# Kernel optimization log

Hardware: AMD Instinct MI355X
Metric: run time of the kernel (lower is better)

Reference implementation:

```python
import jax, jax.numpy as jnp
from jax import lax
import numpy as np

B, C_IN, IMG = 32, 4, 224
FH = FW = IMG // 8  # 28: three stride-2 maxpools
NA = 4
SCORE_T, IOU_T, MAXP = 0.7, 0.3, 10
EPS = 1e-5


def conv2d(x, w, b, pad):
    y = lax.conv_general_dilated(x, w, (1, 1), [(pad, pad), (pad, pad)],
                                 dimension_numbers=('NCHW', 'OIHW', 'NCHW'))
    return y + b[None, :, None, None]


def bn_eval(x, g, b):
    # eval-mode BN with running_mean=0, running_var=1 (fresh model), eps=1e-5
    return x * (g / jnp.sqrt(1.0 + EPS))[None, :, None, None] + b[None, :, None, None]


def maxpool2(x):
    return lax.reduce_window(x, -jnp.inf, lax.max, (1, 1, 2, 2), (1, 1, 2, 2), 'VALID')


def make_anchors():
    ys = (jnp.arange(FH) + 0.5) / FH
    xs = (jnp.arange(FW) + 0.5) / FW
    cy, cx = jnp.meshgrid(ys, xs, indexing='ij')
    cxy = jnp.stack([cx, cy], -1)  # [H,W,2], matches loop order y,x then anchor
    sizes = jnp.array([[16., 16.], [32., 32.], [64., 64.], [128., 128.]], jnp.float32) / 224.0
    a = jnp.concatenate([jnp.broadcast_to(cxy[:, :, None, :], (FH, FW, NA, 2)),
                         jnp.broadcast_to(sizes[None, None], (FH, FW, NA, 2))], -1)
    return a.reshape(-1, 4)  # [H*W*NA, 4] = [3136, 4]


def decode_boxes(anchors, offsets):
    centers = anchors[..., :2] + offsets[..., :2] * 0.1
    sizes = anchors[..., 2:] * jnp.exp(offsets[..., 2:] * 0.2)
    boxes = jnp.concatenate([centers - sizes / 2, centers + sizes / 2], -1)
    return jnp.clip(boxes, 0.0, 1.0)


def nms_single(boxes, scores):
    # greedy NMS, fixed MAXP iterations (== max_proposals_per_image cap)
    N = scores.shape[0]
    s0 = jnp.where(scores > SCORE_T, scores, -jnp.inf)  # score-threshold filter
    areas = (boxes[:, 2] - boxes[:, 0]) * (boxes[:, 3] - boxes[:, 1])
    idx_all = jnp.arange(N)

    def body(s, _):
        i = jnp.argmax(s)
        ok = s[i] > -jnp.inf
        bi = boxes[i]
        xx1 = jnp.maximum(bi[0], boxes[:, 0]); yy1 = jnp.maximum(bi[1], boxes[:, 1])
        xx2 = jnp.minimum(bi[2], boxes[:, 2]); yy2 = jnp.minimum(bi[3], boxes[:, 3])
        inter = jnp.clip(xx2 - xx1, 0.0) * jnp.clip(yy2 - yy1, 0.0)
        iou = inter / (areas[i] + areas - inter)
        sup = (iou > IOU_T) | (idx_all == i)
        s_next = jnp.where(ok & sup, -jnp.inf, s)
        return s_next, (jnp.where(ok, i, 0), ok)

    _, (idxs, oks) = lax.scan(body, s0, None, length=MAXP)
    return idxs, oks  # [MAXP] int32, [MAXP] bool


def _forward(x, r1w, r1b, g1, b1, r2w, r2b, g2, b2, r3w, r3b, g3, b3, rpw, rpb,
             clsw, clsb, regw, regb, c1w, c1b, cg1, cb1, c2w, c2b, cg2, cb2,
             fc1w, fc1b, fc2w, fc2b, fc3w, fc3b, fc4w, fc4b):
    Bsz = x.shape[0]
    # --- Stage 1: lightweight RPN ---
    h = maxpool2(jax.nn.relu(bn_eval(conv2d(x, r1w, r1b, 1), g1, b1)))
    h = maxpool2(jax.nn.relu(bn_eval(conv2d(h, r2w, r2b, 1), g2, b2)))
    h = maxpool2(jax.nn.relu(bn_eval(conv2d(h, r3w, r3b, 1), g3, b3)))
    h = jax.nn.relu(conv2d(h, rpw, rpb, 1))
    cls = conv2d(h, clsw, clsb, 0).transpose(0, 2, 3, 1).reshape(Bsz, -1, 2)
    reg = conv2d(h, regw, regb, 0).transpose(0, 2, 3, 1).reshape(Bsz, -1, 4)
    anchors = make_anchors()
    probs = jax.nn.softmax(cls, -1)[..., 1]        # [B,N] objectness
    boxes = decode_boxes(anchors[None], reg)       # [B,N,4]
    # --- proposal selection: score threshold + greedy NMS + top-10 cap ---
    idxs, oks = jax.vmap(nms_single)(boxes, probs)  # [B,10]
    okf = oks.astype(boxes.dtype)
    kept_boxes = jax.vmap(lambda b, i: b[i])(boxes, idxs) * okf[..., None]
    kept_scores = jax.vmap(lambda s, i: s[i])(probs, idxs) * okf
    has_prop = (probs > SCORE_T).any(-1)           # [B]
    # --- Stage 2: CLM classifier (applied to the full image, as in original) ---
    f = jax.nn.relu(bn_eval(conv2d(x, c1w, c1b, 1), cg1, cb1))
    f = jax.nn.relu(bn_eval(conv2d(f, c2w, c2b, 1), cg2, cb2))
    # AdaptiveAvgPool2d((7,7)) on 224x224 -> mean over 32x32 blocks
    f = f.reshape(Bsz, 128, 7, 32, 7, 32).mean(axis=(3, 5)).reshape(Bsz, -1)
    f = jax.nn.relu(f @ fc1w + fc1b)
    f = jax.nn.relu(f @ fc2w + fc2b)
    f = jax.nn.relu(f @ fc3w + fc3b)
    logits = f @ fc4w + fc4b
    bg = jnp.array([1.0, 0.0], logits.dtype)
    final = jnp.where(has_prop[:, None], logits, bg[None])
    return final, kept_boxes, kept_scores, oks


def setup_inputs() -> dict:
    key = jax.random.key(0)
    ks = iter(jax.random.split(key, 64))

    def conv_w(o, i, k):
        return jax.random.normal(next(ks), (o, i, k, k), jnp.float32) * float(np.sqrt(2.0 / (i * k * k)))

    def lin_w(i, o):
        return jax.random.normal(next(ks), (i, o), jnp.float32) * float(1.0 / np.sqrt(i))

    return {
        'x': jax.random.normal(next(ks), (B, C_IN, IMG, IMG), jnp.float32),
        'r1w': conv_w(32, 4, 3), 'r1b': jnp.zeros(32), 'g1': jnp.ones(32), 'b1': jnp.zeros(32),
        'r2w': conv_w(64, 32, 3), 'r2b': jnp.zeros(64), 'g2': jnp.ones(64), 'b2': jnp.zeros(64),
        'r3w': conv_w(128, 64, 3), 'r3b': jnp.zeros(128), 'g3': jnp.ones(128), 'b3': jnp.zeros(128),
        'rpw': conv_w(256, 128, 3), 'rpb': jnp.zeros(256),
        'clsw': conv_w(8, 256, 1), 'clsb': jnp.zeros(8),
        'regw': conv_w(16, 256, 1), 'regb': jnp.zeros(16),
        'c1w': conv_w(64, 4, 3), 'c1b': jnp.zeros(64), 'cg1': jnp.ones(64), 'cb1': jnp.zeros(64),
        'c2w': conv_w(128, 64, 3), 'c2b': jnp.zeros(128), 'cg2': jnp.ones(128), 'cb2': jnp.zeros(128),
        'fc1w': lin_w(6272, 512), 'fc1b': jnp.zeros(512),
        'fc2w': lin_w(512, 256), 'fc2b': jnp.zeros(256),
        'fc3w': lin_w(256, 128), 'fc3b': jnp.zeros(128),
        'fc4w': lin_w(128, 2), 'fc4b': jnp.zeros(2),
    }


def reference(x, r1w, r1b, g1, b1, r2w, r2b, g2, b2, r3w, r3b, g3, b3, rpw, rpb,
              clsw, clsb, regw, regb, c1w, c1b, cg1, cb1, c2w, c2b, cg2, cb2,
              fc1w, fc1b, fc2w, fc2b, fc3w, fc3b, fc4w, fc4b):
    return _forward(x, r1w, r1b, g1, b1, r2w, r2b, g2, b2, r3w, r3b, g3, b3, rpw, rpb,
                    clsw, clsb, regw, regb, c1w, c1b, cg1, cb1, c2w, c2b, cg2, cb2,
                    fc1w, fc1b, fc2w, fc2b, fc3w, fc3b, fc4w, fc4b)
```

## Files before the change

### kernel.cpp

```cpp
#include <hip/hip_runtime.h>
#include <math.h>

constexpr int NANCH = 3136;
constexpr float SCORE_T = 0.7f;
constexpr float IOU_T = 0.3f;
constexpr int MAXP = 10;

typedef unsigned short u16;
typedef __attribute__((ext_vector_type(8))) short short8x;
typedef __attribute__((ext_vector_type(4))) float f32x4;

__device__ inline u16 f2bf(float f) {
  unsigned u = __builtin_bit_cast(unsigned, f);
  u += 0x7fffu + ((u >> 16) & 1u);
  return (u16)(u >> 16);
}
__device__ inline float bf2f(u16 h) {
  unsigned u = ((unsigned)h) << 16;
  return __builtin_bit_cast(float, u);
}

__global__ __launch_bounds__(256) void w1prep_k(const float* __restrict__ w,
                                                u16* __restrict__ hi, u16* __restrict__ lo,
                                                int COUT) {
  const int i = blockIdx.x * 256 + threadIdx.x;
  if (i >= COUT * 64) return;
  const int k = i & 63, co = i >> 6;
  float v = 0.f;
  if (k < 36) { const int tap = k >> 2, cin = k & 3; v = w[co * 36 + cin * 9 + tap]; }
  const u16 h = f2bf(v);
  hi[i] = h;
  lo[i] = f2bf(v - bf2f(h));
}

template<int MODE>
__global__ __launch_bounds__(256) void c1mfma_k(
    const float* __restrict__ x,
    const u16* __restrict__ wfh, const u16* __restrict__ wfl,
    const float* __restrict__ bias, const float* __restrict__ gamma,
    const float* __restrict__ beta,
    u16* __restrict__ outhi, u16* __restrict__ outlo) {
  constexpr int COUT = MODE ? 32 : 64;
  constexpr int NF   = MODE ? 2 : 4;
  constexpr int PS   = MODE ? 136 : 72;
  __shared__ u16 s_patch[64 * PS];
  __shared__ u16 s_wh[COUT * 72];
  __shared__ u16 s_wl[MODE ? COUT * 72 : 8];
  __shared__ float s_raw[4 * 6 * 18];
  __shared__ float s_pool[MODE ? 4 * 16 * 17 : 1];
  __shared__ u16 s_out[MODE ? 8 : 64 * 72];

  const int tid = threadIdx.x, lane = tid & 63, w = tid >> 6;
  const int lr = lane & 15, lg = lane >> 4;
  const int img = blockIdx.z;
  const int x0 = blockIdx.x * 16, y0 = blockIdx.y * 4;

  for (int i = tid; i < 64 * 7; i += 256) {
    const int p = i / 7, q = i % 7;
    *(uint2*)&s_patch[p * PS + 36 + q * 4] = make_uint2(0, 0);
    if (MODE) *(uint2*)&s_patch[p * PS + 100 + q * 4] = make_uint2(0, 0);
  }
  for (int i = tid; i < 432; i += 256) {
    const int cin = i / 108, r = i % 108;
    const int ry = r / 18, rx = r % 18;
    const int gy = y0 - 1 + ry, gx = x0 - 1 + rx;
    float v = 0.f;
    if ((unsigned)gy < 224u && (unsigned)gx < 224u)
      v = x[(((size_t)img * 4 + cin) * 224 + gy) * 224 + gx];
    s_raw[i] = v;
  }
  for (int i = tid; i < COUT * 8; i += 256) {
    const int co = i >> 3, q = i & 7;
    *(uint4*)&s_wh[co * 72 + q * 8] = *(const uint4*)&wfh[co * 64 + q * 8];
    if (MODE) *(uint4*)&s_wl[co * 72 + q * 8] = *(const uint4*)&wfl[co * 64 + q * 8];
  }
  __syncthreads();

  for (int i = tid; i < 576; i += 256) {
    const int p = i / 9, tap = i % 9;
    const int ty = p >> 4, tx = p & 15;
    const int ky = tap / 3, kx = tap % 3;
    u16 h4[4], l4[4];
#pragma unroll
    for (int cin = 0; cin < 4; cin++) {
      const float v = s_raw[cin * 108 + (ty + ky) * 18 + (tx + kx)];
      h4[cin] = f2bf(v);
      if (MODE) l4[cin] = f2bf(v - bf2f(h4[cin]));
    }
    *(uint2*)&s_patch[p * PS + tap * 4] = *(uint2*)h4;
    if (MODE) *(uint2*)&s_patch[p * PS + 64 + tap * 4] = *(uint2*)l4;
  }
  __syncthreads();

  int pA;
  if (MODE) pA = ((w >> 1) * 2 + (lr >> 3)) * 16 + (w & 1) * 8 + (lr & 7);
  else      pA = w * 16 + lr;

  f32x4 acc[NF];
#pragma unroll
  for (int nf = 0; nf < NF; nf++) acc[nf] = (f32x4)(0.f);

#pragma unroll
  for (int ks = 0; ks < 2; ks++) {
    const short8x ah = *(const short8x*)&s_patch[pA * PS + ks * 32 + lg * 8];
    short8x al;
    if (MODE) al = *(const short8x*)&s_patch[pA * PS + 64 + ks * 32 + lg * 8];
#pragma unroll
    for (int nf = 0; nf < NF; nf++) {
      const short8x bh = *(const short8x*)&s_wh[(nf * 16 + lr) * 72 + ks * 32 + lg * 8];
      if (MODE) {
        const short8x bl = *(const short8x*)&s_wl[(nf * 16 + lr) * 72 + ks * 32 + lg * 8];
        acc[nf] = __builtin_amdgcn_mfma_f32_16x16x32_bf16(al, bh, acc[nf], 0, 0, 0);
        acc[nf] = __builtin_amdgcn_mfma_f32_16x16x32_bf16(ah, bl, acc[nf], 0, 0, 0);
      }
      acc[nf] = __builtin_amdgcn_mfma_f32_16x16x32_bf16(ah, bh, acc[nf], 0, 0, 0);
    }
  }

  const float rsq = 1.f / sqrtf(1.f + 1e-5f);

  if (MODE == 0) {
#pragma unroll
    for (int nf = 0; nf < 4; nf++) {
      const int co = nf * 16 + lr;
      const float bi = bias[co], scl = gamma[co] * rsq, shf = beta[co];
#pragma unroll
      for (int j = 0; j < 4; j++) {
        const float e = fmaxf((acc[nf][j] + bi) * scl + shf, 0.f);
        s_out[(w * 16 + lg * 4 + j) * 72 + co] = f2bf(e);
      }
    }
    __syncthreads();
    for (int i = tid; i < 512; i += 256) {
      const int p = i >> 3, q = i & 7;
      const int oy = y0 + (p >> 4), ox = x0 + (p & 15);
      *(uint4*)&outhi[(((size_t)img * 224 + oy) * 224 + ox) * 64 + q * 8] =
          *(uint4*)&s_out[p * 72 + q * 8];
    }
  } else {
#pragma unroll
    for (int nf = 0; nf < 2; nf++) {
      const int co = nf * 16 + lr;
      const float bi = bias[co], scl = gamma[co] * rsq, shf = beta[co];
#pragma unroll
      for (int j = 0; j < 4; j++) {
        const int m = lg * 4 + j;
        s_pool[w * 272 + m * 17 + lr] = (acc[nf][j] + bi) * scl + shf;
      }
      __syncthreads();
      {
        const int pc = lane >> 4, n = lane & 15;
        const float* sp = &s_pool[w * 272];
        float m0 = fmaxf(sp[(pc * 2) * 17 + n], sp[(pc * 2 + 1) * 17 + n]);
        float m1 = fmaxf(sp[(pc * 2 + 8) * 17 + n], sp[(pc * 2 + 9) * 17 + n]);
        const float mm = fmaxf(fmaxf(m0, m1), 0.f);
        const int py = (y0 >> 1) + (w >> 1), px = (x0 >> 1) + (w & 1) * 4 + pc;
        const size_t o = (((size_t)img * 112 + py) * 112 + px) * 32 + nf * 16 + n;
        const u16 h = f2bf(mm);
        outhi[o] = h; outlo[o] = f2bf(mm - bf2f(h));
      }
      __syncthreads();
    }
  }
}

__global__ __launch_bounds__(256) void wsplit_k(const float* __restrict__ w,
                                                u16* __restrict__ hi, u16* __restrict__ lo,
                                                int COUT, int CIN) {
  const int n = 9 * COUT * CIN;
  const int i = blockIdx.x * 256 + threadIdx.x;
  if (i >= n) return;
  const int cin = i % CIN; int r = i / CIN;
  const int cout = r % COUT; const int tap = r / COUT;
  const float v = w[((size_t)cout * CIN + cin) * 9 + tap];
  const u16 h = f2bf(v);
  hi[i] = h; lo[i] = f2bf(v - bf2f(h));
}

__global__ __launch_bounds__(256) void w2b_k(const float* __restrict__ w,
                                             u16* __restrict__ wb) {
  const int i = blockIdx.x * 256 + threadIdx.x;
  if (i >= 73728) return;
  const int cin = i & 63; const int r = i >> 6;
  const int cout = r & 127; const int tap = r >> 7;
  wb[i] = f2bf(w[(((size_t)cout * 64 + cin) * 3 + tap / 3) * 3 + tap % 3]);
}

template<int CINCH, bool POOL, bool BN>
__global__ __launch_bounds__(256) void sconv_k(
    const u16* __restrict__ ahi, const u16* __restrict__ alo,
    const u16* __restrict__ whi, const u16* __restrict__ wlo,
    const float* __restrict__ bias, const float* __restrict__ gamma,
    const float* __restrict__ beta,
    u16* __restrict__ ohi, u16* __restrict__ olo, float* __restrict__ of32,
    int H, int W, int COUT, int cog) {
  __shared__ u16 s_in[6 * 34 * 72];
  __shared__ u16 s_w[64 * 72];
  const int tid = threadIdx.x, lane = tid & 63, wave = tid >> 6;
  const int wm = wave >> 1, wn = wave & 1, lr = lane & 15, lg = lane >> 4;
  const int img = blockIdx.z / cog, co0 = (blockIdx.z % cog) * 64;
  const int x0 = blockIdx.x * 32, band = blockIdx.y;
  const int CIN = CINCH * 32;

  f32x4 acc[4][2];
#pragma unroll
  for (int mi = 0; mi < 4; ++mi) { acc[mi][0] = (f32x4)(0.f); acc[mi][1] = (f32x4)(0.f); }

  for (int cc2 = 0; cc2 < CINCH; ++cc2) {
    for (int idx = tid; idx < 1632; idx += 256) {
      const int r = idx / 272, rem = idx % 272;
      const int c = rem >> 3, q = rem & 7, pl = q >> 2, qq = q & 3;
      const int gy = band * 4 - 1 + r, gx = x0 - 1 + c;
      uint4 v = make_uint4(0, 0, 0, 0);
      if ((unsigned)gy < (unsigned)H && (unsigned)gx < (unsigned)W) {
        const u16* src = pl ? alo : ahi;
        v = *(const uint4*)(src + ((size_t)(img * H + gy) * W + gx) * CIN + cc2 * 32 + qq * 8);
      }
      *(uint4*)(&s_in[(r * 34 + c) * 72 + pl * 32 + qq * 8]) = v;
    }
    for (int tap = 0; tap < 9; ++tap) {
      const int ky = tap / 3, kx = tap % 3;
      for (int idx = tid; idx < 512; idx += 256) {
        const int cout = idx >> 3, q = idx & 7, pl = q >> 2, qq = q & 3;
        const u16* src = pl ? wlo : whi;
        uint4 v = *(const uint4*)(src + ((size_t)tap * COUT + co0 + cout) * CIN + cc2 * 32 + qq * 8);
        *(uint4*)(&s_w[cout * 72 + pl * 32 + qq * 8]) = v;
      }
      __syncthreads();
      short8x ah[4], al[4], bh[2], bl[2];
#pragma unroll
      for (int mi = 0; mi < 4; ++mi) {
        const int base = ((2 * wm + (mi >> 1) + ky) * 34 + (mi & 1) * 16 + lr + kx) * 72;
        ah[mi] = *(const short8x*)(&s_in[base + lg * 8]);
        al[mi] = *(const short8x*)(&s_in[base + 32 + lg * 8]);
      }
#pragma unroll
      for (int ni = 0; ni < 2; ++ni) {
        const int wb2 = (wn * 32 + ni * 16 + lr) * 72;
        bh[ni] = *(const short8x*)(&s_w[wb2 + lg * 8]);
        bl[ni] = *(const short8x*)(&s_w[wb2 + 32 + lg * 8]);
      }
#pragma unroll
      for (int mi = 0; mi < 4; ++mi)
#pragma unroll
        for (int ni = 0; ni < 2; ++ni) {
          acc[mi][ni] = __builtin_amdgcn_mfma_f32_16x16x32_bf16(al[mi], bh[ni], acc[mi][ni], 0, 0, 0);
          acc[mi][ni] = __builtin_amdgcn_mfma_f32_16x16x32_bf16(ah[mi], bl[ni], acc[mi][ni], 0, 0, 0);
          acc[mi][ni] = __builtin_amdgcn_mfma_f32_16x16x32_bf16(ah[mi], bh[ni], acc[mi][ni], 0, 0, 0);
        }
      __syncthreads();
    }
  }

  const float rsq = 1.f / sqrtf(1.f + 1e-5f);
#pragma unroll
  for (int ni = 0; ni < 2; ++ni) {
    const int cout = co0 + wn * 32 + ni * 16 + lr;
    const float bi = bias[cout];
    const float scl = BN ? gamma[cout] * rsq : 1.f;
    const float shf = BN ? beta[cout] : 0.f;
    if (POOL) {
      const int OH = H >> 1, OW = W >> 1;
      const int py = band * 2 + wm;
#pragma unroll
      for (int ch = 0; ch < 2; ++ch)
#pragma unroll
        for (int jp = 0; jp < 2; ++jp) {
          float m = (acc[ch][ni][2 * jp] + bi) * scl + shf;
          m = fmaxf(m, (acc[ch][ni][2 * jp + 1] + bi) * scl + shf);
          m = fmaxf(m, (acc[ch + 2][ni][2 * jp] + bi) * scl + shf);
          m = fmaxf(m, (acc[ch + 2][ni][2 * jp + 1] + bi) * scl + shf);
          m = fmaxf(m, 0.f);
          const int px = (x0 >> 1) + ch * 8 + lg * 2 + jp;
          if (px < OW) {
            const size_t o = ((size_t)(img * OH + py) * OW + px) * COUT + cout;
            const u16 h = f2bf(m);
            ohi[o] = h; olo[o] = f2bf(m - bf2f(h));
          }
        }
    } else {
#pragma unroll
      for (int mi = 0; mi < 4; ++mi) {
        const int row = band * 4 + 2 * wm + (mi >> 1);
#pragma unroll
        for (int j = 0; j < 4; ++j) {
          const int px = x0 + (mi & 1) * 16 + lg * 4 + j;
          if (px < W)
            of32[((size_t)(img * H + row) * W + px) * COUT + cout] =
                fmaxf(acc[mi][ni][j] + bi, 0.f);
        }
      }
    }
  }
}

__global__ __launch_bounds__(256, 3) void c2band_k(
    const u16* __restrict__ act, const u16* __restrict__ wb,
    const float* __restrict__ bias, const float* __restrict__ gamma,
    const float* __restrict__ beta, float* __restrict__ pooled, int gimg0) {
  __shared__ u16 s_in[6 * 34 * 72];
  __shared__ float s_wp[256];

  const int tid = threadIdx.x;
  const int lane = tid & 63, wave = tid >> 6;
  const int wm = wave >> 1, wn = wave & 1;
  const int lr = lane & 15, lg = lane >> 4;
  const int img = blockIdx.z >> 3, band = blockIdx.z & 7;
  const int x0 = blockIdx.x * 32, y0 = blockIdx.y * 32;
  const float rsq = 1.f / sqrtf(1.f + 1e-5f);

  for (int idx = tid; idx < 1632; idx += 256) {
    const int r = idx / 272, rem = idx % 272;
    const int c = rem >> 3, q = rem & 7;
    const int gy = y0 + band * 4 - 1 + r, gx = x0 - 1 + c;
    uint4 v = make_uint4(0, 0, 0, 0);
    if ((unsigned)gy < 224u && (unsigned)gx < 224u)
      v = *(const uint4*)(act + (((size_t)img * 224 + gy) * 224 + gx) * 64 + q * 8);
    *(uint4*)(&s_in[(r * 34 + c) * 72 + q * 8]) = v;
  }
  __syncthreads();

  f32x4 acc[4][4];
#pragma unroll
  for (int mi = 0; mi < 4; ++mi)
#pragma unroll
    for (int ni = 0; ni < 4; ++ni) acc[mi][ni] = (f32x4)(0.f);

  const u16* wbase = wb + ((size_t)(wn * 64 + lr)) * 64 + lg * 8;

#pragma unroll
  for (int tap = 0; tap < 9; ++tap) {
    const int ky = tap / 3, kx = tap % 3;
    short8x bfr[2][4];
#pragma unroll
    for (int h = 0; h < 2; ++h)
#pragma unroll
      for (int ni = 0; ni < 4; ++ni)
        bfr[h][ni] = *(const short8x*)(wbase + tap * 8192 + ni * 1024 + h * 32);
#pragma unroll
    for (int h = 0; h < 2; ++h) {
      short8x a[4];
#pragma unroll
      for (int mi = 0; mi < 4; ++mi) {
        const int rl = wm * 2 + (mi >> 1) + ky;
        const int cc = (mi & 1) * 16 + lr + kx;
        a[mi] = *(const short8x*)(&s_in[(rl * 34 + cc) * 72 + h * 32 + lg * 8]);
      }
#pragma unroll
      for (int mi = 0; mi < 4; ++mi)
#pragma unroll
        for (int ni = 0; ni < 4; ++ni)
          acc[mi][ni] = __builtin_amdgcn_mfma_f32_16x16x32_bf16(a[mi], bfr[h][ni], acc[mi][ni], 0, 0, 0);
    }
  }

  float part[4];
#pragma unroll
  for (int ni = 0; ni < 4; ++ni) {
    const int co = wn * 64 + ni * 16 + lr;
    const float bi = bias[co], scl = gamma[co] * rsq, shf = beta[co];
    float s = 0.f;
#pragma unroll
    for (int mi = 0; mi < 4; ++mi)
#pragma unroll
      for (int j = 0; j < 4; ++j)
        s += fmaxf((acc[mi][ni][j] + bi) * scl + shf, 0.f);
    s += __shfl_xor(s, 16);
    s += __shfl_xor(s, 32);
    part[ni] = s;
  }
  if (lane < 16) {
#pragma unroll
    for (int ni = 0; ni < 4; ++ni)
      s_wp[wave * 64 + ni * 16 + lr] = part[ni];
  }
  __syncthreads();
  if (tid < 128) {
    const int w0 = tid >> 6, idx = tid & 63;
    const float v = s_wp[w0 * 64 + idx] + s_wp[(w0 + 2) * 64 + idx];
    atomicAdd(&pooled[(size_t)(gimg0 + img) * 6272 + tid * 49 + blockIdx.y * 7 + blockIdx.x],
              v * (1.f / 1024.f));
  }
}

__global__ __launch_bounds__(256) void rpn_head_k(
    const float* __restrict__ feat,
    const float* __restrict__ clsw, const float* __restrict__ clsb,
    const float* __restrict__ regw, const float* __restrict__ regb,
    float* __restrict__ probs, float* __restrict__ boxes) {
  const int gid = blockIdx.x * 256 + threadIdx.x;
  if (gid >= 32 * NANCH) return;
  const int a = gid & 3;
  int r = gid >> 2;
  const int x = r % 28; r /= 28;
  const int y = r % 28;
  const int b = r / 28;

  const float* f = feat + ((size_t)b * 784 + y * 28 + x) * 256;
  float c0 = clsb[2 * a], c1 = clsb[2 * a + 1];
  float r0 = regb[4 * a], r1 = regb[4 * a + 1], r2 = regb[4 * a + 2], r3 = regb[4 * a + 3];
#pragma unroll 4
  for (int c = 0; c < 256; c++) {
    const float fv = f[c];
    c0 = fmaf(fv, clsw[(2 * a) * 256 + c], c0);
    c1 = fmaf(fv, clsw[(2 * a + 1) * 256 + c], c1);
    r0 = fmaf(fv, regw[(4 * a) * 256 + c], r0);
    r1 = fmaf(fv, regw[(4 * a + 1) * 256 + c], r1);
    r2 = fmaf(fv, regw[(4 * a + 2) * 256 + c], r2);
    r3 = fmaf(fv, regw[(4 * a + 3) * 256 + c], r3);
  }
  const float p = 1.f / (1.f + expf(c0 - c1));

  const float cx = (x + 0.5f) * (1.f / 28.f);
  const float cy = (y + 0.5f) * (1.f / 28.f);
  const float sz = (float)(16 << a) * (1.f / 224.f);
  const float ncx = cx + r0 * 0.1f, ncy = cy + r1 * 0.1f;
  const float nw = sz * expf(r2 * 0.2f), nh = sz * expf(r3 * 0.2f);
  const float x1 = fminf(fmaxf(ncx - nw * 0.5f, 0.f), 1.f);
  const float y1 = fminf(fmaxf(ncy - nh * 0.5f, 0.f), 1.f);
  const float x2 = fminf(fmaxf(ncx + nw * 0.5f, 0.f), 1.f);
  const float y2 = fminf(fmaxf(ncy + nh * 0.5f, 0.f), 1.f);

  probs[gid] = p;
  ((float4*)boxes)[gid] = make_float4(x1, y1, x2, y2);
}

__global__ __launch_bounds__(256) void nms_k(
    const float* __restrict__ probs, const float* __restrict__ boxes,
    float* __restrict__ dout, int* __restrict__ hasflag) {
  const int b = blockIdx.x;
  const int t = threadIdx.x;
  __shared__ float sc[NANCH];
  __shared__ float ar[NANCH];
  __shared__ float4 bx[NANCH];
  __shared__ float rv[256];
  __shared__ int   ri[256];
  __shared__ int s_any, s_sel[MAXP], s_ok[MAXP];

  if (t == 0) s_any = 0;
  __syncthreads();

  int anyl = 0;
  for (int i = t; i < NANCH; i += 256) {
    const float p = probs[(size_t)b * NANCH + i];
    const float4 bb = ((const float4*)boxes)[(size_t)b * NANCH + i];
    bx[i] = bb;
    ar[i] = (bb.z - bb.x) * (bb.w - bb.y);
    sc[i] = (p > SCORE_T) ? p : -INFINITY;
    if (p > SCORE_T) anyl = 1;
  }
  if (anyl) atomicOr(&s_any, 1);
  __syncthreads();

  for (int it = 0; it < MAXP; ++it) {
    float bv = -INFINITY; int bi = 0x7fffffff;
    for (int i = t; i < NANCH; i += 256) {
      const float v = sc[i];
      if (v > bv || (v == bv && i < bi)) { bv = v; bi = i; }
    }
    rv[t] = bv; ri[t] = bi;
    __syncthreads();
    for (int st = 128; st > 0; st >>= 1) {
      if (t < st) {
        const float ov = rv[t + st]; const int oi = ri[t + st];
        if (ov > rv[t] || (ov == rv[t] && oi < ri[t])) { rv[t] = ov; ri[t] = oi; }
      }
      __syncthreads();
    }
    if (t == 0) { s_sel[it] = ri[0]; s_ok[it] = (rv[0] > -INFINITY) ? 1 : 0; }
    __syncthreads();
    const int sel = s_sel[it];
    const int ok  = s_ok[it];
    if (ok) {
      const float4 bs = bx[sel]; const float as = ar[sel];
      for (int i = t; i < NANCH; i += 256) {
        const float xx1 = fmaxf(bs.x, bx[i].x), yy1 = fmaxf(bs.y, bx[i].y);
        const float xx2 = fminf(bs.z, bx[i].z), yy2 = fminf(bs.w, bx[i].w);
        const float inter = fmaxf(xx2 - xx1, 0.f) * fmaxf(yy2 - yy1, 0.f);
        const float iou = inter / (as + ar[i] - inter);
        if (iou > IOU_T || i == sel) sc[i] = -INFINITY;
      }
    }
    __syncthreads();
  }

  if (t < MAXP) {
    const int sel = s_ok[t] ? s_sel[t] : 0;
    const float okf = s_ok[t] ? 1.f : 0.f;
    const float4 bb = bx[sel];
    float* kb = dout + 64;
    float* ks = dout + 64 + 32 * MAXP * 4;
    float* ko = dout + 64 + 32 * MAXP * 5;
    const size_t base = ((size_t)b * MAXP + t) * 4;
    kb[base + 0] = bb.x * okf; kb[base + 1] = bb.y * okf;
    kb[base + 2] = bb.z * okf; kb[base + 3] = bb.w * okf;
    ks[b * MAXP + t] = probs[(size_t)b * NANCH + sel] * okf;
    ko[b * MAXP + t] = okf;
  }
  if (t == 0) hasflag[b] = s_any;
}

__global__ __launch_bounds__(64) void fcsplit_k(
    const float* __restrict__ x, const float* __restrict__ w,
    float* __restrict__ part, int K, int N, int kchunk) {
  extern __shared__ float sx[];
  const int o = blockIdx.x * 64 + threadIdx.x;
  const int k0 = blockIdx.y * kchunk;
  for (int i = threadIdx.x; i < 32 * kchunk; i += 64) {
    const int bb = i / kchunk, kk = i % kchunk;
    sx[i] = x[(size_t)bb * K + k0 + kk];
  }
  __syncthreads();
  float acc[32];
#pragma unroll
  for (int bb = 0; bb < 32; bb++) acc[bb] = 0.f;
#pragma unroll 8
  for (int kk = 0; kk < kchunk; kk++) {
    const float wv = w[(size_t)(k0 + kk) * N + o];
#pragma unroll
    for (int bb = 0; bb < 32; bb++) acc[bb] = fmaf(sx[bb * kchunk + kk], wv, acc[bb]);
  }
  float* p = part + (size_t)blockIdx.y * 32 * N + o;
#pragma unroll
  for (int bb = 0; bb < 32; bb++) p[(size_t)bb * N] = acc[bb];
}

__global__ __launch_bounds__(256) void fcreduce_k(
    const float* __restrict__ part, const float* __restrict__ bias,
    float* __restrict__ y, int N, int KT, int dorelu) {
  const int i = blockIdx.x * 256 + threadIdx.x;
  if (i >= 32 * N) return;
  const int o = i % N;
  float s = bias[o];
  for (int kt = 0; kt < KT; kt++) s += part[(size_t)kt * 32 * N + i];
  y[i] = dorelu ? fmaxf(s, 0.f) : s;
}

__global__ __launch_bounds__(64) void final_k(
    const float* __restrict__ f3, const float* __restrict__ w,
    const float* __restrict__ bi, const int* __restrict__ hasflag,
    float* __restrict__ dout) {
  const int t = threadIdx.x;
  if (t >= 64) return;
  const int b = t >> 1, j = t & 1;
  float acc = bi[j];
#pragma unroll 4
  for (int k = 0; k < 128; k++) acc = fmaf(f3[b * 128 + k], w[k * 2 + j], acc);
  dout[b * 2 + j] = hasflag[b] ? acc : (j == 0 ? 1.f : 0.f);
}

extern "C" void kernel_launch(void* const* d_in, const int* in_sizes, int n_in,
                              void* d_out, int out_size, void* d_ws, size_t ws_size,
                              hipStream_t stream) {
  const float* x    = (const float*)d_in[0];
  const float* r1w  = (const float*)d_in[1];  const float* r1b = (const float*)d_in[2];
  const float* g1   = (const float*)d_in[3];  const float* b1  = (const float*)d_in[4];
  const float* r2w  = (const float*)d_in[5];  const float* r2b = (const float*)d_in[6];
  const float* g2   = (const float*)d_in[7];  const float* b2  = (const float*)d_in[8];
  const float* r3w  = (const float*)d_in[9];  const float* r3b = (const float*)d_in[10];
  const float* g3   = (const float*)d_in[11]; const float* b3  = (const float*)d_in[12];
  const float* rpw  = (const float*)d_in[13]; const float* rpb = (const float*)d_in[14];
  const float* clsw = (const float*)d_in[15]; const float* clsb = (const float*)d_in[16];
  const float* regw = (const float*)d_in[17]; const float* regb = (const float*)d_in[18];
  const float* c1w  = (const float*)d_in[19]; const float* c1b = (const float*)d_in[20];
  const float* cg1  = (const float*)d_in[21]; const float* cb1 = (const float*)d_in[22];
  const float* c2w  = (const float*)d_in[23]; const float* c2b = (const float*)d_in[24];
  const float* cg2  = (const float*)d_in[25]; const float* cb2 = (const float*)d_in[26];
  const float* fc1w = (const float*)d_in[27]; const float* fc1b = (const float*)d_in[28];
  const float* fc2w = (const float*)d_in[29]; const float* fc2b = (const float*)d_in[30];
  const float* fc3w = (const float*)d_in[31]; const float* fc3b = (const float*)d_in[32];
  const float* fc4w = (const float*)d_in[33]; const float* fc4b = (const float*)d_in[34];
  float* dout = (float*)d_out;
  float* Wp = (float*)d_ws;

  const size_t o_h1   = 0;
  const size_t o_h2   = 12845056;
  const size_t o_h3   = o_h2 + 6422528;
  const size_t o_prob = o_h3 + 3211264;
  const size_t o_box  = o_prob + 100352;
  const size_t o_flag = o_box + 401408;
  const size_t o_pool = o_flag + 32;
  const size_t o_f1   = o_pool + 200704;
  const size_t o_f2   = o_f1 + 16384;
  const size_t o_f3   = o_f2 + 8192;
  const size_t o_w2b  = o_f3 + 4096;
  const size_t o_w2s  = o_w2b + 36864;
  const size_t o_w3s  = o_w2s + 18432;
  const size_t o_wps  = o_w3s + 73728;
  const size_t o_w1r  = o_wps + 294912;
  const size_t o_w1c  = o_w1r + 2048;

  u16* h1hi = (u16*)(Wp + o_h1); u16* h1lo = h1hi + 12845056;
  u16* h2hi = (u16*)(Wp + o_h2); u16* h2lo = h2hi + 6422528;
  u16* h3hi = (u16*)(Wp + o_h3); u16* h3lo = h3hi + 3211264;
  float* probs = Wp + o_prob; float* boxes = Wp + o_box;
  int* hasflag = (int*)(Wp + o_flag);
  float* pooled = Wp + o_pool;
  float* f1 = Wp + o_f1; float* f2 = Wp + o_f2; float* f3 = Wp + o_f3;
  u16* w2b  = (u16*)(Wp + o_w2b);
  u16* w2hi = (u16*)(Wp + o_w2s); u16* w2lo = w2hi + 18432;
  u16* w3hi = (u16*)(Wp + o_w3s); u16* w3lo = w3hi + 73728;
  u16* wphi = (u16*)(Wp + o_wps); u16* wplo = wphi + 294912;
  u16* w1rhi = (u16*)(Wp + o_w1r); u16* w1rlo = w1rhi + 2048;
  u16* w1chi = (u16*)(Wp + o_w1c); u16* w1clo = w1chi + 4096;
  float* h4f32 = Wp + o_h1;
  u16*   c1buf = (u16*)(Wp + o_h1);
  float* fcpart = Wp + o_h1;

  wsplit_k<<<(9 * 64 * 32 + 255) / 256, 256, 0, stream>>>(r2w, w2hi, w2lo, 64, 32);
  wsplit_k<<<(9 * 128 * 64 + 255) / 256, 256, 0, stream>>>(r3w, w3hi, w3lo, 128, 64);
  wsplit_k<<<(9 * 256 * 128 + 255) / 256, 256, 0, stream>>>(rpw, wphi, wplo, 256, 128);
  w2b_k<<<288, 256, 0, stream>>>(c2w, w2b);
  w1prep_k<<<8, 256, 0, stream>>>(r1w, w1rhi, w1rlo, 32);
  w1prep_k<<<16, 256, 0, stream>>>(c1w, w1chi, w1clo, 64);

  c1mfma_k<1><<<dim3(14, 56, 32), 256, 0, stream>>>(
      x, w1rhi, w1rlo, r1b, g1, b1, h1hi, h1lo);
  sconv_k<1, true, true><<<dim3(4, 28, 32), 256, 0, stream>>>(
      h1hi, h1lo, w2hi, w2lo, r2b, g2, b2, h2hi, h2lo, nullptr, 112, 112, 64, 1);
  sconv_k<2, true, true><<<dim3(2, 14, 64), 256, 0, stream>>>(
      h2hi, h2lo, w3hi, w3lo, r3b, g3, b3, h3hi, h3lo, nullptr, 56, 56, 128, 2);
  sconv_k<4, false, false><<<dim3(1, 7, 128), 256, 0, stream>>>(
      h3hi, h3lo, wphi, wplo, rpb, rpb, rpb, nullptr, nullptr, h4f32, 28, 28, 256, 4);

  rpn_head_k<<<(32 * NANCH + 255) / 256, 256, 0, stream>>>(h4f32, clsw, clsb, regw, regb, probs, boxes);
  nms_k<<<32, 256, 0, stream>>>(probs, boxes, dout, hasflag);

  hipMemsetAsync(pooled, 0, 32 * 6272 * sizeof(float), stream);
  constexpr int CHUNK = 8;
  for (int c0 = 0; c0 < 32; c0 += CHUNK) {
    c1mfma_k<0><<<dim3(14, 56, CHUNK), 256, 0, stream>>>(
        x + (size_t)c0 * 4 * 224 * 224, w1chi, w1clo, c1b, cg1, cb1, c1buf, nullptr);
    c2band_k<<<dim3(7, 7, CHUNK * 8), 256, 0, stream>>>(
        c1buf, w2b, c2b, cg2, cb2, pooled, c0);
  }

  fcsplit_k<<<dim3(8, 64), 64, 32 * 98 * 4, stream>>>(pooled, fc1w, fcpart, 6272, 512, 98);
  fcreduce_k<<<64, 256, 0, stream>>>(fcpart, fc1b, f1, 512, 64, 1);
  fcsplit_k<<<dim3(4, 16), 64, 32 * 32 * 4, stream>>>(f1, fc2w, fcpart, 512, 256, 32);
  fcreduce_k<<<32, 256, 0, stream>>>(fcpart, fc2b, f2, 256, 16, 1);
  fcsplit_k<<<dim3(2, 8), 64, 32 * 32 * 4, stream>>>(f2, fc3w, fcpart, 256, 128, 32);
  fcreduce_k<<<16, 256, 0, stream>>>(fcpart, fc3b, f3, 128, 8, 1);
  final_k<<<1, 64, 0, stream>>>(f3, fc4w, fc4b, hasflag, dout);
}
```

Measured before the change: 1.371 ms.

## Stage conv2 weights through double-buffered LDS with register prefetch

In the conv2 band kernel, each tap's weight slice is no longer read straight from global memory by every wave. The block now loads it cooperatively into a padded, double-buffered shared-memory tile, prefetching the next tap into registers while the current tap's MFMAs run. The goal is to cut redundant global/L2 weight traffic and hide load latency. In exchange it adds about 40KB of LDS and a barrier per tap, and lowers the occupancy bound from 3 to 2 blocks per CU.

```diff
diff --git a/kernel.cpp b/kernel.cpp
--- a/kernel.cpp
+++ b/kernel.cpp
@@ -294,11 +294,12 @@
   }
 }
 
-__global__ __launch_bounds__(256, 3) void c2band_k(
+__global__ __launch_bounds__(256, 2) void c2band_k(
     const u16* __restrict__ act, const u16* __restrict__ wb,
     const float* __restrict__ bias, const float* __restrict__ gamma,
     const float* __restrict__ beta, float* __restrict__ pooled, int gimg0) {
   __shared__ u16 s_in[6 * 34 * 72];
+  __shared__ u16 s_w[2][2 * 128 * 40];
   __shared__ float s_wp[256];
 
   const int tid = threadIdx.x;
@@ -318,6 +319,25 @@
       v = *(const uint4*)(act + (((size_t)img * 224 + gy) * 224 + gx) * 64 + q * 8);
     *(uint4*)(&s_in[(r * 34 + c) * 72 + q * 8]) = v;
   }
+
+  uint4 wreg0, wreg1, wreg2, wreg3;
+  const int i0 = tid, i1 = tid + 256, i2 = tid + 512, i3 = tid + 768;
+#define WLOAD(tap)                                                          \
+  {                                                                         \
+    wreg0 = *(const uint4*)(wb + ((size_t)(tap) * 128 + (i0 >> 3)) * 64 + (i0 & 7) * 8); \
+    wreg1 = *(const uint4*)(wb + ((size_t)(tap) * 128 + (i1 >> 3)) * 64 + (i1 & 7) * 8); \
+    wreg2 = *(const uint4*)(wb + ((size_t)(tap) * 128 + (i2 >> 3)) * 64 + (i2 & 7) * 8); \
+    wreg3 = *(const uint4*)(wb + ((size_t)(tap) * 128 + (i3 >> 3)) * 64 + (i3 & 7) * 8); \
+  }
+#define WSTORE(buf)                                                         \
+  {                                                                         \
+    *(uint4*)(&s_w[buf][((i0 & 7) >> 2) * 5120 + (i0 >> 3) * 40 + (i0 & 3) * 8]) = wreg0; \
+    *(uint4*)(&s_w[buf][((i1 & 7) >> 2) * 5120 + (i1 >> 3) * 40 + (i1 & 3) * 8]) = wreg1; \
+    *(uint4*)(&s_w[buf][((i2 & 7) >> 2) * 5120 + (i2 >> 3) * 40 + (i2 & 3) * 8]) = wreg2; \
+    *(uint4*)(&s_w[buf][((i3 & 7) >> 2) * 5120 + (i3 >> 3) * 40 + (i3 & 3) * 8]) = wreg3; \
+  }
+
+  WLOAD(0); WSTORE(0);
   __syncthreads();
 
   f32x4 acc[4][4];
@@ -326,20 +346,14 @@
 #pragma unroll
     for (int ni = 0; ni < 4; ++ni) acc[mi][ni] = (f32x4)(0.f);
 
-  const u16* wbase = wb + ((size_t)(wn * 64 + lr)) * 64 + lg * 8;
-
 #pragma unroll
   for (int tap = 0; tap < 9; ++tap) {
+    const int cur = tap & 1;
+    if (tap < 8) WLOAD(tap + 1);
     const int ky = tap / 3, kx = tap % 3;
-    short8x bfr[2][4];
-#pragma unroll
-    for (int h = 0; h < 2; ++h)
-#pragma unroll
-      for (int ni = 0; ni < 4; ++ni)
-        bfr[h][ni] = *(const short8x*)(wbase + tap * 8192 + ni * 1024 + h * 32);
 #pragma unroll
     for (int h = 0; h < 2; ++h) {
-      short8x a[4];
+      short8x a[4], bf[4];
 #pragma unroll
       for (int mi = 0; mi < 4; ++mi) {
         const int rl = wm * 2 + (mi >> 1) + ky;
@@ -347,12 +361,21 @@
         a[mi] = *(const short8x*)(&s_in[(rl * 34 + cc) * 72 + h * 32 + lg * 8]);
       }
 #pragma unroll
+      for (int ni = 0; ni < 4; ++ni) {
+        const int co = wn * 64 + ni * 16 + lr;
+        bf[ni] = *(const short8x*)(&s_w[cur][h * 5120 + co * 40 + lg * 8]);
+      }
+#pragma unroll
       for (int mi = 0; mi < 4; ++mi)
 #pragma unroll
         for (int ni = 0; ni < 4; ++ni)
-          acc[mi][ni] = __builtin_amdgcn_mfma_f32_16x16x32_bf16(a[mi], bfr[h][ni], acc[mi][ni], 0, 0, 0);
-    }
-  }
+          acc[mi][ni] = __builtin_amdgcn_mfma_f32_16x16x32_bf16(a[mi], bf[ni], acc[mi][ni], 0, 0, 0);
+    }
+    if (tap < 8) WSTORE(cur ^ 1);
+    __syncthreads();
+  }
+#undef WLOAD
+#undef WSTORE
 
   float part[4];
 #pragma unroll
```

Measured after the change: 1.098 ms. 20.0% less time.
